# Optimization experiments

Measured on AMD Instinct MI355X. Metric: run time of the kernel, lower is better.

Reference implementation:

```python
import jax, jax.numpy as jnp
import numpy as np

N = 100000
E = 3200000
IN_DIM, HID, RED, EMB = 2, 64, 32, 32
LN_EPS = 1e-5


def gcn_conv(x, W, b, row, col, w_full, dinv):
    # x:[N,F_in] W:[F_in,F_out]; PyG GCNConv: lin (no bias) -> normalized scatter-add -> + bias
    xw = x @ W                                  # [N,F_out]
    norm = dinv[row] * w_full * dinv[col]       # [E+N]
    msgs = norm[:, None] * xw[row]              # gather from source nodes
    out = jax.ops.segment_sum(msgs, col, num_segments=N)
    return out + b


def layer_norm(x, g, b):
    mu = jnp.mean(x, axis=-1, keepdims=True)
    var = jnp.mean((x - mu) ** 2, axis=-1, keepdims=True)
    return (x - mu) * jax.lax.rsqrt(var + LN_EPS) * g + b


def setup_inputs() -> dict:
    key = jax.random.key(0)
    ks = jax.random.split(key, 12)
    def glorot(k, shape):
        lim = float(np.sqrt(6.0 / (shape[0] + shape[1])))
        return jax.random.uniform(k, shape, jnp.float32, -lim, lim)
    return {
        "x": jax.random.normal(ks[0], (N, IN_DIM), jnp.float32),
        "edge_weight": jax.random.uniform(ks[1], (E,), jnp.float32),
        "W1": glorot(ks[2], (IN_DIM, HID)), "b1": jnp.zeros((HID,), jnp.float32),
        "rW1": glorot(ks[3], (IN_DIM, HID)), "rb1": jnp.zeros((HID,), jnp.float32),
        "g1": jnp.ones((HID,), jnp.float32), "be1": jnp.zeros((HID,), jnp.float32),
        "W2": glorot(ks[4], (HID, RED)), "b2": jnp.zeros((RED,), jnp.float32),
        "rW2": glorot(ks[5], (HID, RED)), "rb2": jnp.zeros((RED,), jnp.float32),
        "g2": jnp.ones((RED,), jnp.float32), "be2": jnp.zeros((RED,), jnp.float32),
        "fcW": glorot(ks[6], (RED, 1)), "fcb": jnp.zeros((1,), jnp.float32),
        "pW": glorot(ks[7], (RED, EMB)), "pb": jnp.zeros((EMB,), jnp.float32),
        "edge_index": jax.random.randint(ks[8], (2, E), 0, N, jnp.int64)
        if jax.config.read("jax_enable_x64") else jax.random.randint(ks[8], (2, E), 0, N, jnp.int32),
    }


def reference(x, edge_weight, W1, b1, rW1, rb1, g1, be1, W2, b2, rW2, rb2, g2, be2,
              fcW, fcb, pW, pb, edge_index):
    row, col = edge_index[0], edge_index[1]
    # add self-loops with weight 1 (PyG gcn_norm default)
    loops = jnp.arange(N, dtype=row.dtype)
    row_f = jnp.concatenate([row, loops])
    col_f = jnp.concatenate([col, loops])
    w_f = jnp.concatenate([edge_weight, jnp.ones((N,), edge_weight.dtype)])
    deg = jax.ops.segment_sum(w_f, col_f, num_segments=N)
    dinv = jnp.where(deg > 0, jax.lax.rsqrt(jnp.where(deg > 0, deg, 1.0)), 0.0)

    x1 = gcn_conv(x, W1, b1, row_f, col_f, w_f, dinv) + (x @ rW1 + rb1)
    x1 = jax.nn.relu(layer_norm(x1, g1, be1))
    x2 = gcn_conv(x1, W2, b2, row_f, col_f, w_f, dinv) + (x1 @ rW2 + rb2)
    x2 = jax.nn.relu(layer_norm(x2, g2, be2))

    logits = (x2 @ fcW + fcb)[:, 0]
    proj = x2 @ pW + pb
    nrm = jnp.linalg.norm(proj, axis=1, keepdims=True)
    emb = proj / jnp.maximum(nrm, 1e-12)
    return logits, emb
```

## Files before the change

kernel.cpp:

```cpp
#include <hip/hip_runtime.h>
#include <hip/hip_bf16.h>

#define NN 100000
#define NE 3200000
#define LN_EPS 1e-5f
#define NBUCK 196
#define TILE 4096
#define NTILE 782
#define CAP 20480
#define L1NB 16

__global__ void k_ginit(int* __restrict__ gcur) {
    int b = threadIdx.x;
    if (b < NBUCK) gcur[b] = b * CAP;
}

__global__ __launch_bounds__(256) void k_partA(
        const int* __restrict__ row, const int* __restrict__ col,
        const float* __restrict__ w, int* __restrict__ gcur,
        int2* __restrict__ tmp) {
    __shared__ int2 sbuf[TILE];
    __shared__ int  gpos[TILE];
    __shared__ int  lhist[NBUCK];
    __shared__ int  lofs[NBUCK];
    __shared__ int  lbase[NBUCK];
    __shared__ int  wsum[4];
    int t = threadIdx.x;
    long base_e = (long)blockIdx.x * TILE;
    int nt = NE - base_e < TILE ? (int)(NE - base_e) : TILE;

    for (int b = t; b < NBUCK; b += 256) lhist[b] = 0;
    __syncthreads();

    int pk[16]; float wv16[16]; int bri[16];
    #pragma unroll
    for (int i = 0; i < 16; ++i) {
        int j = t + i * 256;
        if (j < nt) {
            int e = (int)base_e + j;
            int r = row[e], c = col[e];
            pk[i] = r | ((c & 511) << 17);
            wv16[i] = w[e];
            int b = c >> 9;
            int rk = atomicAdd(&lhist[b], 1);
            bri[i] = (b << 16) | rk;
        } else bri[i] = -1;
    }
    __syncthreads();

    {
        int v = (t < NBUCK) ? lhist[t] : 0;
        int lane = t & 63;
        int inc = v;
        #pragma unroll
        for (int off = 1; off < 64; off <<= 1) {
            int u = __shfl_up(inc, off, 64);
            if (lane >= off) inc += u;
        }
        if (lane == 63) wsum[t >> 6] = inc;
        __syncthreads();
        int wv = t >> 6;
        int woff = 0;
        for (int j = 0; j < 4; ++j) if (j < wv) woff += wsum[j];
        if (t < NBUCK) {
            lofs[t] = woff + inc - v;
            lbase[t] = atomicAdd(&gcur[t], v);
        }
    }
    __syncthreads();

    #pragma unroll
    for (int i = 0; i < 16; ++i) {
        if (bri[i] >= 0) {
            int b = bri[i] >> 16, rk = bri[i] & 0xFFFF;
            int slot = lofs[b] + rk;
            sbuf[slot] = make_int2(pk[i], __float_as_int(wv16[i]));
            gpos[slot] = lbase[b] + rk;
        }
    }
    __syncthreads();

    #pragma unroll
    for (int i = 0; i < 16; ++i) {
        int j = t + i * 256;
        if (j < nt) tmp[gpos[j]] = sbuf[j];
    }
}

__global__ void k_cscan(const int* __restrict__ gcur, int* __restrict__ obase,
                        int* __restrict__ ptr) {
    __shared__ int sm[256];
    int t = threadIdx.x;
    int v = (t < NBUCK) ? (gcur[t] - t * CAP) : 0;
    sm[t] = v;
    __syncthreads();
    for (int off = 1; off < 256; off <<= 1) {
        int u = (t >= off) ? sm[t - off] : 0;
        __syncthreads();
        sm[t] += u;
        __syncthreads();
    }
    if (t < NBUCK) obase[t] = sm[t] - v;
    if (t == 0) ptr[NN] = NE;
}

__global__ __launch_bounds__(1024) void k_partB1(
        const int* __restrict__ gcur, const int* __restrict__ obase,
        const int2* __restrict__ tmp, const float* __restrict__ x,
        int* __restrict__ ptr, float* __restrict__ dinv, float2* __restrict__ y) {
    __shared__ int   nh[512];
    __shared__ float wsumf[512];
    __shared__ int   wscan[8];
    int b = blockIdx.x;
    int t = threadIdx.x;
    int start = b * CAP, end = gcur[b];
    int cnt = end - start;
    int outb = obase[b];
    if (t < 512) { nh[t] = 0; wsumf[t] = 0.0f; }
    __syncthreads();
    const int4* tp = (const int4*)(tmp + start);
    int npair = cnt >> 1;
    for (int p = t; p < npair; p += 1024) {
        int4 rr = tp[p];
        int cl0 = ((unsigned)rr.x) >> 17;
        atomicAdd(&nh[cl0], 1);
        atomicAdd(&wsumf[cl0], __int_as_float(rr.y));
        int cl1 = ((unsigned)rr.z) >> 17;
        atomicAdd(&nh[cl1], 1);
        atomicAdd(&wsumf[cl1], __int_as_float(rr.w));
    }
    if ((cnt & 1) && t == 0) {
        int2 rec = tmp[end - 1];
        int cl = ((unsigned)rec.x) >> 17;
        atomicAdd(&nh[cl], 1);
        atomicAdd(&wsumf[cl], __int_as_float(rec.y));
    }
    __syncthreads();
    int v = 0, inc = 0;
    if (t < 512) {
        v = nh[t];
        inc = v;
        #pragma unroll
        for (int off = 1; off < 64; off <<= 1) {
            int u = __shfl_up(inc, off, 64);
            if ((t & 63) >= off) inc += u;
        }
        if ((t & 63) == 63) wscan[t >> 6] = inc;
    }
    __syncthreads();
    if (t < 512) {
        int wv = t >> 6;
        int woff = 0;
        #pragma unroll
        for (int j = 0; j < 8; ++j) if (j < wv) woff += wscan[j];
        int ex = outb + woff + inc - v;
        int gn = b * 512 + t;
        if (gn < NN) {
            ptr[gn] = ex;
            float di = rsqrtf(wsumf[t] + 1.0f);
            dinv[gn] = di;
            float2 xv = *(const float2*)(x + 2 * gn);
            y[gn] = make_float2(di * xv.x, di * xv.y);
        }
    }
}

__global__ __launch_bounds__(1024) void k_partB2(
        const int* __restrict__ gcur, const int2* __restrict__ tmp,
        const int* __restrict__ ptr, const float* __restrict__ dinv,
        const float2* __restrict__ y,
        unsigned* __restrict__ csrp, float* __restrict__ agg1) {
    __shared__ int   nh[512];
    __shared__ float a0s[512];
    __shared__ float a1s[512];
    int b = blockIdx.x;
    int t = threadIdx.x;
    int start = b * CAP, end = gcur[b];
    int cnt = end - start;
    if (t < 512) {
        int gn = b * 512 + t;
        nh[t] = (gn < NN) ? ptr[gn] : 0;
        a0s[t] = 0.0f; a1s[t] = 0.0f;
    }
    __syncthreads();
    const int4* tp = (const int4*)(tmp + start);
    int npair = cnt >> 1;
    for (int p = t; p < npair; p += 1024) {
        int4 rr = tp[p];
        {
            int cl = ((unsigned)rr.x) >> 17;
            int r = rr.x & 0x1FFFF;
            float wf = __int_as_float(rr.y);
            __hip_bfloat16 hb = __float2bfloat16(wf);
            unsigned short wbits = *reinterpret_cast<unsigned short*>(&hb);
            int pos = atomicAdd(&nh[cl], 1);
            csrp[pos] = ((unsigned)r << 15) | (unsigned)wbits;
            float2 yv = y[r];
            atomicAdd(&a0s[cl], wf * yv.x);
            atomicAdd(&a1s[cl], wf * yv.y);
        }
        {
            int cl = ((unsigned)rr.z) >> 17;
            int r = rr.z & 0x1FFFF;
            float wf = __int_as_float(rr.w);
            __hip_bfloat16 hb = __float2bfloat16(wf);
            unsigned short wbits = *reinterpret_cast<unsigned short*>(&hb);
            int pos = atomicAdd(&nh[cl], 1);
            csrp[pos] = ((unsigned)r << 15) | (unsigned)wbits;
            float2 yv = y[r];
            atomicAdd(&a0s[cl], wf * yv.x);
            atomicAdd(&a1s[cl], wf * yv.y);
        }
    }
    if ((cnt & 1) && t == 0) {
        int2 rec = tmp[end - 1];
        int cl = ((unsigned)rec.x) >> 17;
        int r = rec.x & 0x1FFFF;
        float wf = __int_as_float(rec.y);
        __hip_bfloat16 hb = __float2bfloat16(wf);
        unsigned short wbits = *reinterpret_cast<unsigned short*>(&hb);
        int pos = atomicAdd(&nh[cl], 1);
        csrp[pos] = ((unsigned)r << 15) | (unsigned)wbits;
        float2 yv = y[r];
        atomicAdd(&a0s[cl], wf * yv.x);
        atomicAdd(&a1s[cl], wf * yv.y);
    }
    __syncthreads();
    if (t < 512) {
        int gn = b * 512 + t;
        if (gn < NN) {
            float di = dinv[gn];
            float2 yv = y[gn];
            agg1[2 * gn]     = di * (a0s[t] + yv.x);
            agg1[2 * gn + 1] = di * (a1s[t] + yv.y);
        }
    }
}

__global__ __launch_bounds__(256) void k_l1t2(
        const float* __restrict__ agg1, const float* __restrict__ x,
        const float* __restrict__ dinv,
        const float* __restrict__ W1, const float* __restrict__ b1,
        const float* __restrict__ rW1, const float* __restrict__ rb1,
        const float* __restrict__ g1, const float* __restrict__ be1,
        const float* __restrict__ W2, const float* __restrict__ b2,
        const float* __restrict__ rW2, const float* __restrict__ rb2,
        __hip_bfloat16* __restrict__ t2, float* __restrict__ agg2i) {
    __shared__ float wT[64][68];
    __shared__ float xs[L1NB][68];
    int tid = threadIdx.x;
    for (int i = tid; i < 4096; i += 256) {
        int j = i >> 6, o = i & 63;
        wT[o][j] = (o < 32) ? W2[j * 32 + o] : rW2[j * 32 + (o - 32)];
    }
    int wid = tid >> 6, lane = tid & 63;
    int base = blockIdx.x * L1NB;
    float w10 = W1[lane], w11 = W1[64 + lane];
    float r10 = rW1[lane], r11 = rW1[64 + lane];
    float bb = b1[lane] + rb1[lane];
    float gg = g1[lane], be = be1[lane];
    #pragma unroll
    for (int sub = 0; sub < 4; ++sub) {
        int n = base + wid * 4 + sub;
        float a0 = agg1[2 * n], a1 = agg1[2 * n + 1];
        float xa = x[2 * n], xb = x[2 * n + 1];
        float v = a0 * w10 + a1 * w11 + xa * r10 + xb * r11 + bb;
        float s = v;
        #pragma unroll
        for (int m = 32; m >= 1; m >>= 1) s += __shfl_xor(s, m, 64);
        float mean = s * (1.0f / 64.0f);
        float e = v - mean;
        float s2 = e * e;
        #pragma unroll
        for (int m = 32; m >= 1; m >>= 1) s2 += __shfl_xor(s2, m, 64);
        float var = s2 * (1.0f / 64.0f);
        xs[wid * 4 + sub][lane] = fmaxf(e * rsqrtf(var + LN_EPS) * gg + be, 0.0f);
    }
    __syncthreads();
    int o = lane, g = wid;
    const float4* wrow = (const float4*)&wT[o][0];
    const float4* x0 = (const float4*)&xs[g][0];
    const float4* x1r = (const float4*)&xs[g + 4][0];
    const float4* x2r = (const float4*)&xs[g + 8][0];
    const float4* x3r = (const float4*)&xs[g + 12][0];
    float acc0 = 0.0f, acc1 = 0.0f, acc2 = 0.0f, acc3 = 0.0f;
    #pragma unroll
    for (int jq = 0; jq < 16; ++jq) {
        float4 wv = wrow[jq];
        float4 a = x0[jq], b = x1r[jq], c = x2r[jq], d = x3r[jq];
        acc0 += wv.x * a.x + wv.y * a.y + wv.z * a.z + wv.w * a.w;
        acc1 += wv.x * b.x + wv.y * b.y + wv.z * b.z + wv.w * b.w;
        acc2 += wv.x * c.x + wv.y * c.y + wv.z * c.z + wv.w * c.w;
        acc3 += wv.x * d.x + wv.y * d.y + wv.z * d.z + wv.w * d.w;
    }
    float res0 = __shfl_xor(acc0, 32, 64);
    float res1 = __shfl_xor(acc1, 32, 64);
    float res2 = __shfl_xor(acc2, 32, 64);
    float res3 = __shfl_xor(acc3, 32, 64);
    if (o < 32) {
        float accs[4] = {acc0, acc1, acc2, acc3};
        float ress[4] = {res0, res1, res2, res3};
        #pragma unroll
        for (int i = 0; i < 4; ++i) {
            int n = base + g + 4 * i;
            float di = dinv[n];
            t2[n * 32 + o] = __float2bfloat16(accs[i] * di);
            agg2i[n * 32 + o] = accs[i] * di * di + b2[o] + ress[i] + rb2[o];
        }
    }
}

__global__ __launch_bounds__(256) void k_agg2fin(
        const int* __restrict__ ptr, const unsigned* __restrict__ csrp,
        const float* __restrict__ dinv, const __hip_bfloat16* __restrict__ t2,
        const float* __restrict__ agg2i,
        const float* __restrict__ g2, const float* __restrict__ be2,
        const float* __restrict__ fcW, const float* __restrict__ fcb,
        const float* __restrict__ pW, const float* __restrict__ pb,
        float* __restrict__ out) {
    int node = (blockIdx.x * blockDim.x + threadIdx.x) >> 5;
    int l = threadIdx.x & 31;
    if (node >= NN) return;
    int sub = l >> 4, k2 = l & 15;
    int start = ptr[node], n = ptr[node + 1] - start;
    const unsigned* t2u = (const unsigned*)t2;
    float ax = 0.0f, ay = 0.0f;
    int j16 = n & ~15;
    for (int j = 0; j < j16; j += 16) {
        uint4 pa = *(const uint4*)(csrp + start + j);
        uint4 pb4 = *(const uint4*)(csrp + start + j + 4);
        uint4 pc = *(const uint4*)(csrp + start + j + 8);
        uint4 pd = *(const uint4*)(csrp + start + j + 12);
        unsigned p0 = sub ? pa.y : pa.x;
        unsigned p1 = sub ? pa.w : pa.z;
        unsigned p2 = sub ? pb4.y : pb4.x;
        unsigned p3 = sub ? pb4.w : pb4.z;
        unsigned p4 = sub ? pc.y : pc.x;
        unsigned p5 = sub ? pc.w : pc.z;
        unsigned p6 = sub ? pd.y : pd.x;
        unsigned p7 = sub ? pd.w : pd.z;
        unsigned u0 = t2u[(p0 >> 15) * 16 + k2];
        unsigned u1 = t2u[(p1 >> 15) * 16 + k2];
        unsigned u2 = t2u[(p2 >> 15) * 16 + k2];
        unsigned u3 = t2u[(p3 >> 15) * 16 + k2];
        unsigned u4 = t2u[(p4 >> 15) * 16 + k2];
        unsigned u5 = t2u[(p5 >> 15) * 16 + k2];
        unsigned u6 = t2u[(p6 >> 15) * 16 + k2];
        unsigned u7 = t2u[(p7 >> 15) * 16 + k2];
        float w0 = __uint_as_float((p0 & 0x7FFFu) << 16);
        float w1 = __uint_as_float((p1 & 0x7FFFu) << 16);
        float w2 = __uint_as_float((p2 & 0x7FFFu) << 16);
        float w3 = __uint_as_float((p3 & 0x7FFFu) << 16);
        float w4 = __uint_as_float((p4 & 0x7FFFu) << 16);
        float w5 = __uint_as_float((p5 & 0x7FFFu) << 16);
        float w6 = __uint_as_float((p6 & 0x7FFFu) << 16);
        float w7 = __uint_as_float((p7 & 0x7FFFu) << 16);
        ax += w0 * __uint_as_float(u0 << 16) + w1 * __uint_as_float(u1 << 16)
            + w2 * __uint_as_float(u2 << 16) + w3 * __uint_as_float(u3 << 16)
            + w4 * __uint_as_float(u4 << 16) + w5 * __uint_as_float(u5 << 16)
            + w6 * __uint_as_float(u6 << 16) + w7 * __uint_as_float(u7 << 16);
        ay += w0 * __uint_as_float(u0 & 0xFFFF0000u) + w1 * __uint_as_float(u1 & 0xFFFF0000u)
            + w2 * __uint_as_float(u2 & 0xFFFF0000u) + w3 * __uint_as_float(u3 & 0xFFFF0000u)
            + w4 * __uint_as_float(u4 & 0xFFFF0000u) + w5 * __uint_as_float(u5 & 0xFFFF0000u)
            + w6 * __uint_as_float(u6 & 0xFFFF0000u) + w7 * __uint_as_float(u7 & 0xFFFF0000u);
    }
    int j8 = n & ~7;
    for (int j = j16; j < j8; j += 8) {
        uint4 pa = *(const uint4*)(csrp + start + j);
        uint4 pb4 = *(const uint4*)(csrp + start + j + 4);
        unsigned p0 = sub ? pa.y : pa.x;
        unsigned p1 = sub ? pa.w : pa.z;
        unsigned p2 = sub ? pb4.y : pb4.x;
        unsigned p3 = sub ? pb4.w : pb4.z;
        unsigned u0 = t2u[(p0 >> 15) * 16 + k2];
        unsigned u1 = t2u[(p1 >> 15) * 16 + k2];
        unsigned u2 = t2u[(p2 >> 15) * 16 + k2];
        unsigned u3 = t2u[(p3 >> 15) * 16 + k2];
        float w0 = __uint_as_float((p0 & 0x7FFFu) << 16);
        float w1 = __uint_as_float((p1 & 0x7FFFu) << 16);
        float w2 = __uint_as_float((p2 & 0x7FFFu) << 16);
        float w3 = __uint_as_float((p3 & 0x7FFFu) << 16);
        ax += w0 * __uint_as_float(u0 << 16) + w1 * __uint_as_float(u1 << 16)
            + w2 * __uint_as_float(u2 << 16) + w3 * __uint_as_float(u3 << 16);
        ay += w0 * __uint_as_float(u0 & 0xFFFF0000u) + w1 * __uint_as_float(u1 & 0xFFFF0000u)
            + w2 * __uint_as_float(u2 & 0xFFFF0000u) + w3 * __uint_as_float(u3 & 0xFFFF0000u);
    }
    for (int j = j8; j < n; ++j) {
        unsigned p = csrp[start + j];
        float wf = (sub == 0) ? __uint_as_float((p & 0x7FFFu) << 16) : 0.0f;
        unsigned u = t2u[(p >> 15) * 16 + k2];
        ax += wf * __uint_as_float(u << 16);
        ay += wf * __uint_as_float(u & 0xFFFF0000u);
    }
    ax += __shfl_xor(ax, 16, 32);
    ay += __shfl_xor(ay, 16, 32);
    float di = dinv[node];
    float2 ai = ((const float2*)(agg2i + node * 32))[k2];
    float v0 = ai.x + di * ax;
    float v1 = ai.y + di * ay;
    float s = v0 + v1;
    #pragma unroll
    for (int m = 8; m >= 1; m >>= 1) s += __shfl_xor(s, m, 32);
    float mean = s * (1.0f / 32.0f);
    float e0 = v0 - mean, e1 = v1 - mean;
    float s2 = e0 * e0 + e1 * e1;
    #pragma unroll
    for (int m = 8; m >= 1; m >>= 1) s2 += __shfl_xor(s2, m, 32);
    float rstd = rsqrtf(s2 * (1.0f / 32.0f) + LN_EPS);
    float2 gv = ((const float2*)g2)[k2];
    float2 bv = ((const float2*)be2)[k2];
    float x0 = fmaxf(e0 * rstd * gv.x + bv.x, 0.0f);
    float x1 = fmaxf(e1 * rstd * gv.y + bv.y, 0.0f);
    float2 fv = ((const float2*)fcW)[k2];
    float lg = x0 * fv.x + x1 * fv.y;
    #pragma unroll
    for (int m = 8; m >= 1; m >>= 1) lg += __shfl_xor(lg, m, 32);
    if (l == 0) out[node] = lg + fcb[0];
    int o = l;
    float acc2 = pb[o];
    #pragma unroll
    for (int j = 0; j < 16; ++j) {
        float xa = __shfl(x0, j, 32);
        float xb = __shfl(x1, j, 32);
        acc2 += xa * pW[(2 * j) * 32 + o] + xb * pW[(2 * j + 1) * 32 + o];
    }
    float n2 = acc2 * acc2;
    #pragma unroll
    for (int m = 16; m >= 1; m >>= 1) n2 += __shfl_xor(n2, m, 32);
    float nrm = sqrtf(n2);
    out[NN + node * 32 + o] = acc2 / fmaxf(nrm, 1e-12f);
}

extern "C" void kernel_launch(void* const* d_in, const int* in_sizes, int n_in,
                              void* d_out, int out_size, void* d_ws, size_t ws_size,
                              hipStream_t stream) {
    const float* x   = (const float*)d_in[0];
    const float* ew  = (const float*)d_in[1];
    const float* W1  = (const float*)d_in[2];
    const float* b1  = (const float*)d_in[3];
    const float* rW1 = (const float*)d_in[4];
    const float* rb1 = (const float*)d_in[5];
    const float* g1  = (const float*)d_in[6];
    const float* be1 = (const float*)d_in[7];
    const float* W2  = (const float*)d_in[8];
    const float* b2  = (const float*)d_in[9];
    const float* rW2 = (const float*)d_in[10];
    const float* rb2 = (const float*)d_in[11];
    const float* g2  = (const float*)d_in[12];
    const float* be2 = (const float*)d_in[13];
    const float* fcW = (const float*)d_in[14];
    const float* fcb = (const float*)d_in[15];
    const float* pW  = (const float*)d_in[16];
    const float* pb  = (const float*)d_in[17];
    const int*   ei  = (const int*)d_in[18];
    const int* row = ei;
    const int* col = ei + NE;

    char* p = (char*)d_ws;
    unsigned* csrp = (unsigned*)p;            p += (size_t)NE * 4;
    char* regionA = p;                        p += (size_t)NBUCK * CAP * 8;
    __hip_bfloat16* t2 = (__hip_bfloat16*)regionA;
    float* agg2i = (float*)(regionA + (size_t)NN * 32 * 2);
    int2*  tmp   = (int2*)regionA;
    float* dinv  = (float*)p;                 p += (size_t)NN * 4;
    float2* y    = (float2*)p;                p += (size_t)NN * 8;
    float* agg1  = (float*)p;                 p += (size_t)2 * NN * 4;
    int*   ptr   = (int*)p;                   p += (size_t)(NN + 1) * 4;
    int*   gcur  = (int*)p;                   p += 256 * 4;
    int*   obase = (int*)p;                   p += 256 * 4;

    float* out = (float*)d_out;
    const int TB = 256;
    const int NODE32 = (NN * 32 + TB - 1) / TB;

    k_ginit<<<1, 256, 0, stream>>>(gcur);
    k_partA<<<NTILE, 256, 0, stream>>>(row, col, ew, gcur, tmp);
    k_cscan<<<1, 256, 0, stream>>>(gcur, obase, ptr);
    k_partB1<<<NBUCK, 1024, 0, stream>>>(gcur, obase, tmp, x, ptr, dinv, y);
    k_partB2<<<NBUCK, 1024, 0, stream>>>(gcur, tmp, ptr, dinv, y, csrp, agg1);
    k_l1t2<<<NN / L1NB, 256, 0, stream>>>(agg1, x, dinv, W1, b1, rW1, rb1, g1, be1,
                                          W2, b2, rW2, rb2, t2, agg2i);
    k_agg2fin<<<NODE32, TB, 0, stream>>>(ptr, csrp, dinv, t2, agg2i,
                                         g2, be2, fcW, fcb, pW, pb, out);
}
```

Before: 223.3 us.

## Enlarge layer-1 node tile, compact partition scatter index, nontemporal CSR loads

The fused layer-1/layer-2-linear kernel now handles 80 nodes per block instead of 16, so the 64x64 transposed weight tile staged in shared memory is loaded once for five times as many nodes, at the cost of 20 accumulators per thread and more register pressure. The edge partition kernel stores a one-byte bucket id per slot instead of a full global position and rebuilds the destination from lbase and lofs, which shrinks shared memory. The layer-2 aggregation streams CSR entries with nontemporal loads so they are less likely to displace the gathered bf16 features from cache.

New measurement: 703.0 us. 3.15x slower.

```diff
diff --git a/kernel.cpp b/kernel.cpp
--- a/kernel.cpp
+++ b/kernel.cpp
@@ -8,7 +8,9 @@
 #define TILE 4096
 #define NTILE 782
 #define CAP 20480
-#define L1NB 16
+#define L1NB 80
+
+typedef unsigned uv4 __attribute__((ext_vector_type(4)));
 
 __global__ void k_ginit(int* __restrict__ gcur) {
     int b = threadIdx.x;
@@ -20,7 +22,7 @@
         const float* __restrict__ w, int* __restrict__ gcur,
         int2* __restrict__ tmp) {
     __shared__ int2 sbuf[TILE];
-    __shared__ int  gpos[TILE];
+    __shared__ unsigned char bid[TILE];
     __shared__ int  lhist[NBUCK];
     __shared__ int  lofs[NBUCK];
     __shared__ int  lbase[NBUCK];
@@ -75,7 +77,7 @@
             int b = bri[i] >> 16, rk = bri[i] & 0xFFFF;
             int slot = lofs[b] + rk;
             sbuf[slot] = make_int2(pk[i], __float_as_int(wv16[i]));
-            gpos[slot] = lbase[b] + rk;
+            bid[slot] = (unsigned char)b;
         }
     }
     __syncthreads();
@@ -83,7 +85,10 @@
     #pragma unroll
     for (int i = 0; i < 16; ++i) {
         int j = t + i * 256;
-        if (j < nt) tmp[gpos[j]] = sbuf[j];
+        if (j < nt) {
+            int b = bid[j];
+            tmp[lbase[b] + (j - lofs[b])] = sbuf[j];
+        }
     }
 }
 
@@ -259,9 +264,9 @@
     float r10 = rW1[lane], r11 = rW1[64 + lane];
     float bb = b1[lane] + rb1[lane];
     float gg = g1[lane], be = be1[lane];
-    #pragma unroll
-    for (int sub = 0; sub < 4; ++sub) {
-        int n = base + wid * 4 + sub;
+    #pragma unroll 4
+    for (int sub = 0; sub < 20; ++sub) {
+        int n = base + wid * 20 + sub;
         float a0 = agg1[2 * n], a1 = agg1[2 * n + 1];
         float xa = x[2 * n], xb = x[2 * n + 1];
         float v = a0 * w10 + a1 * w11 + xa * r10 + xb * r11 + bb;
@@ -274,38 +279,31 @@
         #pragma unroll
         for (int m = 32; m >= 1; m >>= 1) s2 += __shfl_xor(s2, m, 64);
         float var = s2 * (1.0f / 64.0f);
-        xs[wid * 4 + sub][lane] = fmaxf(e * rsqrtf(var + LN_EPS) * gg + be, 0.0f);
-    }
-    __syncthreads();
-    int o = lane, g = wid;
+        xs[wid * 20 + sub][lane] = fmaxf(e * rsqrtf(var + LN_EPS) * gg + be, 0.0f);
+    }
+    __syncthreads();
+    int o = lane;
     const float4* wrow = (const float4*)&wT[o][0];
-    const float4* x0 = (const float4*)&xs[g][0];
-    const float4* x1r = (const float4*)&xs[g + 4][0];
-    const float4* x2r = (const float4*)&xs[g + 8][0];
-    const float4* x3r = (const float4*)&xs[g + 12][0];
-    float acc0 = 0.0f, acc1 = 0.0f, acc2 = 0.0f, acc3 = 0.0f;
+    float acc[20];
+    #pragma unroll
+    for (int i = 0; i < 20; ++i) acc[i] = 0.0f;
     #pragma unroll
     for (int jq = 0; jq < 16; ++jq) {
         float4 wv = wrow[jq];
-        float4 a = x0[jq], b = x1r[jq], c = x2r[jq], d = x3r[jq];
-        acc0 += wv.x * a.x + wv.y * a.y + wv.z * a.z + wv.w * a.w;
-        acc1 += wv.x * b.x + wv.y * b.y + wv.z * b.z + wv.w * b.w;
-        acc2 += wv.x * c.x + wv.y * c.y + wv.z * c.z + wv.w * c.w;
-        acc3 += wv.x * d.x + wv.y * d.y + wv.z * d.z + wv.w * d.w;
-    }
-    float res0 = __shfl_xor(acc0, 32, 64);
-    float res1 = __shfl_xor(acc1, 32, 64);
-    float res2 = __shfl_xor(acc2, 32, 64);
-    float res3 = __shfl_xor(acc3, 32, 64);
-    if (o < 32) {
-        float accs[4] = {acc0, acc1, acc2, acc3};
-        float ress[4] = {res0, res1, res2, res3};
-        #pragma unroll
-        for (int i = 0; i < 4; ++i) {
-            int n = base + g + 4 * i;
+        #pragma unroll
+        for (int i = 0; i < 20; ++i) {
+            float4 a = ((const float4*)&xs[wid + 4 * i][0])[jq];
+            acc[i] += wv.x * a.x + wv.y * a.y + wv.z * a.z + wv.w * a.w;
+        }
+    }
+    #pragma unroll
+    for (int i = 0; i < 20; ++i) {
+        float res = __shfl_xor(acc[i], 32, 64);
+        if (o < 32) {
+            int n = base + wid + 4 * i;
             float di = dinv[n];
-            t2[n * 32 + o] = __float2bfloat16(accs[i] * di);
-            agg2i[n * 32 + o] = accs[i] * di * di + b2[o] + ress[i] + rb2[o];
+            t2[n * 32 + o] = __float2bfloat16(acc[i] * di);
+            agg2i[n * 32 + o] = acc[i] * di * di + b2[o] + res + rb2[o];
         }
     }
 }
@@ -327,18 +325,18 @@
     float ax = 0.0f, ay = 0.0f;
     int j16 = n & ~15;
     for (int j = 0; j < j16; j += 16) {
-        uint4 pa = *(const uint4*)(csrp + start + j);
-        uint4 pb4 = *(const uint4*)(csrp + start + j + 4);
-        uint4 pc = *(const uint4*)(csrp + start + j + 8);
-        uint4 pd = *(const uint4*)(csrp + start + j + 12);
-        unsigned p0 = sub ? pa.y : pa.x;
-        unsigned p1 = sub ? pa.w : pa.z;
-        unsigned p2 = sub ? pb4.y : pb4.x;
-        unsigned p3 = sub ? pb4.w : pb4.z;
-        unsigned p4 = sub ? pc.y : pc.x;
-        unsigned p5 = sub ? pc.w : pc.z;
-        unsigned p6 = sub ? pd.y : pd.x;
-        unsigned p7 = sub ? pd.w : pd.z;
+        uv4 pa = __builtin_nontemporal_load((const uv4*)(csrp + start + j));
+        uv4 pb4 = __builtin_nontemporal_load((const uv4*)(csrp + start + j + 4));
+        uv4 pc = __builtin_nontemporal_load((const uv4*)(csrp + start + j + 8));
+        uv4 pd = __builtin_nontemporal_load((const uv4*)(csrp + start + j + 12));
+        unsigned p0 = sub ? pa[1] : pa[0];
+        unsigned p1 = sub ? pa[3] : pa[2];
+        unsigned p2 = sub ? pb4[1] : pb4[0];
+        unsigned p3 = sub ? pb4[3] : pb4[2];
+        unsigned p4 = sub ? pc[1] : pc[0];
+        unsigned p5 = sub ? pc[3] : pc[2];
+        unsigned p6 = sub ? pd[1] : pd[0];
+        unsigned p7 = sub ? pd[3] : pd[2];
         unsigned u0 = t2u[(p0 >> 15) * 16 + k2];
         unsigned u1 = t2u[(p1 >> 15) * 16 + k2];
         unsigned u2 = t2u[(p2 >> 15) * 16 + k2];
@@ -366,12 +364,12 @@
     }
     int j8 = n & ~7;
     for (int j = j16; j < j8; j += 8) {
-        uint4 pa = *(const uint4*)(csrp + start + j);
-        uint4 pb4 = *(const uint4*)(csrp + start + j + 4);
-        unsigned p0 = sub ? pa.y : pa.x;
-        unsigned p1 = sub ? pa.w : pa.z;
-        unsigned p2 = sub ? pb4.y : pb4.x;
-        unsigned p3 = sub ? pb4.w : pb4.z;
+        uv4 pa = __builtin_nontemporal_load((const uv4*)(csrp + start + j));
+        uv4 pb4 = __builtin_nontemporal_load((const uv4*)(csrp + start + j + 4));
+        unsigned p0 = sub ? pa[1] : pa[0];
+        unsigned p1 = sub ? pa[3] : pa[2];
+        unsigned p2 = sub ? pb4[1] : pb4[0];
+        unsigned p3 = sub ? pb4[3] : pb4[2];
         unsigned u0 = t2u[(p0 >> 15) * 16 + k2];
         unsigned u1 = t2u[(p1 >> 15) * 16 + k2];
         unsigned u2 = t2u[(p2 >> 15) * 16 + k2];
```
